# Kernel optimization log

Hardware: AMD Instinct MI355X
Metric: run time of the kernel (lower is better)

## Reference

```python
import jax, jax.numpy as jnp
import numpy as np


def setup_inputs() -> dict:
    key = jax.random.key(0)
    k1, k2, k3 = jax.random.split(key, 3)
    B, N, D = 16, 4096, 64
    q = jax.random.normal(k1, (B, N, D), dtype=jnp.float32)
    k = jax.random.normal(k2, (B, N, D), dtype=jnp.float32)
    v = jax.random.normal(k3, (B, N, D), dtype=jnp.float32)
    return {"q": q, "k": k, "v": v}


def reference(q, k, v):
    # attention = softmax(q @ k^T, axis=2)  (scale=None in the torch module,
    # dropout=0.0 is identity)
    scores = jnp.einsum("bnd,bmd->bnm", q, k)          # [B, N, N]
    attention = jax.nn.softmax(scores, axis=2)          # softmax over keys
    context = jnp.einsum("bnm,bmd->bnd", attention, v)  # [B, N, D]
    return (context, attention)
```

## Files before the change

kernel.cpp:

```cpp
#include <hip/hip_runtime.h>
#include <hip/hip_bf16.h>

typedef _Float16 half8 __attribute__((ext_vector_type(8)));
typedef _Float16 half4 __attribute__((ext_vector_type(4)));
typedef short short8 __attribute__((ext_vector_type(8)));
typedef short short4v __attribute__((ext_vector_type(4)));
typedef float f32x4 __attribute__((ext_vector_type(4)));

#define BATCH 16
#define SEQ   4096
#define DIM   64
#define KVB   64
#define NCH   (SEQ / KVB)
#define NSC   (NCH / 2)
#define EL_CH 4096
#define EL_SC 8192
#define EL_B  (NCH * EL_CH)
#define PHS   136

__device__ __forceinline__ short f2bf(float f) {
    unsigned u = __builtin_bit_cast(unsigned, f);
    u += 0x7FFF + ((u >> 16) & 1);
    return (short)(u >> 16);
}
__device__ __forceinline__ float bf2f(short h) {
    return __builtin_bit_cast(float, (unsigned)((unsigned short)h) << 16);
}

__device__ __forceinline__ void gld16(const void* g, void* l) {
    __builtin_amdgcn_global_load_lds(
        (const __attribute__((address_space(1))) unsigned int*)g,
        (__attribute__((address_space(3))) unsigned int*)l, 16, 0, 0);
}

__global__ __launch_bounds__(256) void preconvert(
    const float* __restrict__ k, const float* __restrict__ v,
    _Float16* __restrict__ kh, _Float16* __restrict__ vh)
{
    int f = blockIdx.x * 256 + threadIdx.x;
    int lane = f & 63;
    int sub  = (f >> 6) & 7;
    int ch   = (f >> 9) & 63;
    int bb   = (f >> 15) & 15;
    int isV  = f >> 19;
    int nf = sub >> 1, kk = sub & 1;
    size_t fo = (size_t)(f & ((1 << 19) - 1)) * 8;

    if (!isV) {
        int key = ch * 64 + nf * 16 + (lane & 15);
        int d0  = kk * 32 + (lane >> 4) * 8;
        const float* src = k + (((size_t)bb * SEQ + key) * DIM + d0);
        half8 h8;
        #pragma unroll
        for (int e = 0; e < 8; ++e) h8[e] = (_Float16)src[e];
        *(half8*)(kh + fo) = h8;
    } else {
        int kr0 = kk * 32 + (lane >> 4) * 8;
        int d   = nf * 16 + (lane & 15);
        const float* src = v + (((size_t)bb * SEQ + ch * 64 + kr0) * DIM + d);
        half8 h8;
        #pragma unroll
        for (int e = 0; e < 8; ++e) h8[e] = (_Float16)src[e * DIM];
        *(half8*)(vh + fo) = h8;
    }
}

__global__ __launch_bounds__(512, 2) void attn_main(
    const float* __restrict__ q, const _Float16* __restrict__ kh,
    const _Float16* __restrict__ vh, float* __restrict__ ctx,
    float* __restrict__ att)
{
    __shared__ __align__(16) _Float16 Kst[2][EL_SC];
    __shared__ __align__(16) _Float16 Vst[2][EL_SC];
    __shared__ __align__(16) _Float16 Ph[8][16][PHS];

    int id = blockIdx.x;
    int bb = (id & 7) + 8 * (id >> 8);
    int qt = (id >> 3) & 31;

    int tid = threadIdx.x;
    int w = tid >> 6, lane = tid & 63, li = lane & 15, h4 = lane >> 4;

    int qrow = qt * 128 + w * 16 + li;
    const float* qp = q + ((size_t)bb * SEQ + qrow) * DIM;
    half8 aq[2];
    #pragma unroll
    for (int kk = 0; kk < 2; ++kk)
        #pragma unroll
        for (int e = 0; e < 8; ++e)
            aq[kk][e] = (_Float16)qp[kk * 32 + h4 * 8 + e];

    const _Float16* khb = kh + (size_t)bb * EL_B;
    const _Float16* vvb = vh + (size_t)bb * EL_B;

    auto qkt = [&](const _Float16* base, f32x4* s) {
        const half8* k8 = (const half8*)base;
        #pragma unroll
        for (int kk = 0; kk < 2; ++kk)
            #pragma unroll
            for (int nf = 0; nf < 4; ++nf)
                s[nf] = __builtin_amdgcn_mfma_f32_16x16x32_f16(
                    k8[(nf * 2 + kk) * 64 + lane], aq[kk], s[nf], 0, 0, 0);
    };

    float ll = 0.f;

    auto stage_sc = [&](int buf, int sc) {
        const _Float16* g = khb + (size_t)sc * EL_SC + tid * 8;
        gld16(g,        &Kst[buf][w * 512]);
        gld16(g + 4096, &Kst[buf][4096 + w * 512]);
    };

    stage_sc(0, 0);
    for (int sc = 0; sc < NSC; ++sc) {
        int buf = sc & 1;
        if (sc + 1 < NSC) {
            stage_sc(buf ^ 1, sc + 1);
            asm volatile("s_waitcnt vmcnt(2)" ::: "memory");
        } else {
            asm volatile("s_waitcnt vmcnt(0)" ::: "memory");
        }
        __builtin_amdgcn_s_barrier();
        asm volatile("" ::: "memory");

        #pragma unroll
        for (int c2 = 0; c2 < 2; ++c2) {
            f32x4 s[4];
            #pragma unroll
            for (int nf = 0; nf < 4; ++nf) s[nf] = (f32x4){0.f, 0.f, 0.f, 0.f};
            qkt(&Kst[buf][c2 * EL_CH], s);
            float a = 0.f;
            #pragma unroll
            for (int nf = 0; nf < 4; ++nf)
                #pragma unroll
                for (int r = 0; r < 4; ++r)
                    a += __expf(s[nf][r]);
            ll += a;
        }

        asm volatile("" ::: "memory");
        __builtin_amdgcn_s_barrier();
    }

    ll += __shfl_xor(ll, 16);
    ll += __shfl_xor(ll, 32);
    float rl = 1.0f / ll;

    f32x4 acc[4];
    #pragma unroll
    for (int nf = 0; nf < 4; ++nf) acc[nf] = (f32x4){0.f, 0.f, 0.f, 0.f};

    float* attb = att + ((size_t)bb * SEQ + (size_t)qt * 128 + w * 16) * SEQ;

    auto stage_k2 = [&](int buf, int sc) {
        const _Float16* g = khb + (size_t)sc * EL_SC + tid * 8;
        gld16(g,        &Kst[buf][w * 512]);
        gld16(g + 4096, &Kst[buf][4096 + w * 512]);
    };
    auto stage_v2 = [&](int buf, int sc) {
        const _Float16* g = vvb + (size_t)sc * EL_SC + tid * 8;
        gld16(g,        &Vst[buf][w * 512]);
        gld16(g + 4096, &Vst[buf][4096 + w * 512]);
    };

    stage_k2(0, 0); stage_v2(0, 0);
    for (int sc = 0; sc < NSC; ++sc) {
        int buf = sc & 1;
        if (sc + 1 < NSC) {
            stage_k2(buf ^ 1, sc + 1);
            stage_v2(buf ^ 1, sc + 1);
            if (sc == 0) asm volatile("s_waitcnt vmcnt(4)"  ::: "memory");
            else         asm volatile("s_waitcnt vmcnt(12)" ::: "memory");
        } else {
            asm volatile("s_waitcnt vmcnt(8)" ::: "memory");
        }
        __builtin_amdgcn_s_barrier();
        asm volatile("" ::: "memory");

        f32x4 sA[4], sB[4];
        #pragma unroll
        for (int nf = 0; nf < 4; ++nf) {
            sA[nf] = (f32x4){0.f, 0.f, 0.f, 0.f};
            sB[nf] = (f32x4){0.f, 0.f, 0.f, 0.f};
        }
        qkt(&Kst[buf][0],     sA);
        qkt(&Kst[buf][EL_CH], sB);

        #pragma unroll
        for (int nf = 0; nf < 4; ++nf) {
            half4 pa, pb;
            #pragma unroll
            for (int r = 0; r < 4; ++r) {
                pa[r] = (_Float16)(__expf(sA[nf][r]) * rl);
                pb[r] = (_Float16)(__expf(sB[nf][r]) * rl);
            }
            *(half4*)&Ph[w][li][nf * 16 + h4 * 4]      = pa;
            *(half4*)&Ph[w][li][64 + nf * 16 + h4 * 4] = pb;
        }

        #pragma unroll
        for (int j = 0; j < 4; ++j) {
            int row = j * 4 + h4;
            half4 pa = *(const half4*)&Ph[w][row][li * 4];
            half4 pb = *(const half4*)&Ph[w][row][64 + li * 4];
            f32x4 va = { (float)pa[0], (float)pa[1], (float)pa[2], (float)pa[3] };
            f32x4 vb = { (float)pb[0], (float)pb[1], (float)pb[2], (float)pb[3] };
            float* dst = attb + (size_t)row * SEQ + sc * 128;
            __builtin_nontemporal_store(va, (f32x4*)(dst + li * 4));
            __builtin_nontemporal_store(vb, (f32x4*)(dst + 64 + li * 4));
        }

        const half8* v8 = (const half8*)&Vst[buf][0];
        #pragma unroll
        for (int kk = 0; kk < 4; ++kk) {
            half8 pa = *(const half8*)&Ph[w][li][kk * 32 + h4 * 8];
            #pragma unroll
            for (int nf = 0; nf < 4; ++nf)
                acc[nf] = __builtin_amdgcn_mfma_f32_16x16x32_f16(
                    pa, v8[(kk >> 1) * 512 + (nf * 2 + (kk & 1)) * 64 + lane],
                    acc[nf], 0, 0, 0);
        }

        asm volatile("" ::: "memory");
        __builtin_amdgcn_s_barrier();
    }

    float* ctxb = ctx + ((size_t)bb * SEQ + (size_t)qt * 128 + w * 16) * DIM;
    #pragma unroll
    for (int nf = 0; nf < 4; ++nf)
        #pragma unroll
        for (int r = 0; r < 4; ++r)
            __builtin_nontemporal_store(
                acc[nf][r], &ctxb[(size_t)(4 * h4 + r) * DIM + nf * 16 + li]);
}

__global__ __launch_bounds__(256) void attn_fallback(
    const float* __restrict__ q, const float* __restrict__ k,
    const float* __restrict__ v, float* __restrict__ ctx,
    float* __restrict__ att)
{
    __shared__ short K_hi[KVB][72];
    __shared__ short K_lo[KVB][72];
    __shared__ short V_lds[DIM][72];
    __shared__ short P_lds[4][16][72];

    int id = blockIdx.x;
    int bb = (id & 7) + 8 * (id >> 9);
    int qt = (id >> 3) & 63;
    int tid = threadIdx.x;
    int w = tid >> 6, lane = tid & 63, li = lane & 15, h4 = lane >> 4;

    int qrow = qt * 64 + w * 16 + li;
    const float* qp = q + ((size_t)bb * SEQ + qrow) * DIM;
    short8 aq[2], aql[2];
    #pragma unroll
    for (int kk = 0; kk < 2; ++kk)
        #pragma unroll
        for (int e = 0; e < 8; ++e) {
            float x = qp[kk * 32 + h4 * 8 + e];
            short h = f2bf(x);
            aq[kk][e] = h; aql[kk][e] = f2bf(x - bf2f(h));
        }

    float m[4], l[4];
    #pragma unroll
    for (int r = 0; r < 4; ++r) { m[r] = -3.0e38f; l[r] = 0.0f; }
    const float* kbase = k + (size_t)bb * SEQ * DIM;
    const float* vbase = v + (size_t)bb * SEQ * DIM;

    for (int ch = 0; ch < NCH; ++ch) {
        __syncthreads();
        const float4* kc = (const float4*)(kbase + (size_t)ch * KVB * DIM);
        #pragma unroll
        for (int j = 0; j < 4; ++j) {
            int f4 = j * 256 + tid; int key = f4 >> 4, d4 = f4 & 15;
            float4 val = kc[f4];
            short4v h4v, l4v;
            h4v[0]=f2bf(val.x); l4v[0]=f2bf(val.x-bf2f(h4v[0]));
            h4v[1]=f2bf(val.y); l4v[1]=f2bf(val.y-bf2f(h4v[1]));
            h4v[2]=f2bf(val.z); l4v[2]=f2bf(val.z-bf2f(h4v[2]));
            h4v[3]=f2bf(val.w); l4v[3]=f2bf(val.w-bf2f(h4v[3]));
            *(short4v*)&K_hi[key][d4*4] = h4v;
            *(short4v*)&K_lo[key][d4*4] = l4v;
        }
        __syncthreads();
        f32x4 s[4];
        #pragma unroll
        for (int nf = 0; nf < 4; ++nf) s[nf] = (f32x4){0.f,0.f,0.f,0.f};
        #pragma unroll
        for (int kk = 0; kk < 2; ++kk)
            #pragma unroll
            for (int nf = 0; nf < 4; ++nf) {
                short8 kbv = *(const short8*)&K_hi[nf*16+li][kk*32+h4*8];
                short8 klv = *(const short8*)&K_lo[nf*16+li][kk*32+h4*8];
                s[nf] = __builtin_amdgcn_mfma_f32_16x16x32_bf16(aq[kk],  kbv, s[nf],0,0,0);
                s[nf] = __builtin_amdgcn_mfma_f32_16x16x32_bf16(aq[kk],  klv, s[nf],0,0,0);
                s[nf] = __builtin_amdgcn_mfma_f32_16x16x32_bf16(aql[kk], kbv, s[nf],0,0,0);
            }
        #pragma unroll
        for (int r = 0; r < 4; ++r) {
            float cmax = fmaxf(fmaxf(s[0][r],s[1][r]), fmaxf(s[2][r],s[3][r]));
            #pragma unroll
            for (int off = 1; off < 16; off <<= 1) cmax = fmaxf(cmax, __shfl_xor(cmax, off));
            float mnew = fmaxf(m[r], cmax);
            float cs = __expf(s[0][r]-mnew)+__expf(s[1][r]-mnew)+__expf(s[2][r]-mnew)+__expf(s[3][r]-mnew);
            #pragma unroll
            for (int off = 1; off < 16; off <<= 1) cs += __shfl_xor(cs, off);
            l[r] = l[r]*__expf(m[r]-mnew) + cs; m[r] = mnew;
        }
    }
    float rl[4];
    #pragma unroll
    for (int r = 0; r < 4; ++r) rl[r] = 1.0f / l[r];

    f32x4 acc[4];
    #pragma unroll
    for (int nf = 0; nf < 4; ++nf) acc[nf] = (f32x4){0.f,0.f,0.f,0.f};
    float* attb = att + ((size_t)bb * SEQ + (size_t)qt * 64 + w * 16) * SEQ;

    for (int ch = 0; ch < NCH; ++ch) {
        __syncthreads();
        const float4* kc = (const float4*)(kbase + (size_t)ch * KVB * DIM);
        #pragma unroll
        for (int j = 0; j < 4; ++j) {
            int f4 = j * 256 + tid; int key = f4 >> 4, d4 = f4 & 15;
            float4 val = kc[f4];
            short4v h4v, l4v;
            h4v[0]=f2bf(val.x); l4v[0]=f2bf(val.x-bf2f(h4v[0]));
            h4v[1]=f2bf(val.y); l4v[1]=f2bf(val.y-bf2f(h4v[1]));
            h4v[2]=f2bf(val.z); l4v[2]=f2bf(val.z-bf2f(h4v[2]));
            h4v[3]=f2bf(val.w); l4v[3]=f2bf(val.w-bf2f(h4v[3]));
            *(short4v*)&K_hi[key][d4*4] = h4v;
            *(short4v*)&K_lo[key][d4*4] = l4v;
        }
        {
            int key = tid & 63, dblk = (tid >> 6) * 16;
            const float* vc = vbase + ((size_t)ch * KVB + key) * DIM + dblk;
            #pragma unroll
            for (int j = 0; j < 4; ++j) {
                float4 val = *(const float4*)(vc + j * 4);
                V_lds[dblk+j*4+0][key]=f2bf(val.x); V_lds[dblk+j*4+1][key]=f2bf(val.y);
                V_lds[dblk+j*4+2][key]=f2bf(val.z); V_lds[dblk+j*4+3][key]=f2bf(val.w);
            }
        }
        __syncthreads();
        f32x4 s[4];
        #pragma unroll
        for (int nf = 0; nf < 4; ++nf) s[nf] = (f32x4){0.f,0.f,0.f,0.f};
        #pragma unroll
        for (int kk = 0; kk < 2; ++kk)
            #pragma unroll
            for (int nf = 0; nf < 4; ++nf) {
                short8 kbv = *(const short8*)&K_hi[nf*16+li][kk*32+h4*8];
                short8 klv = *(const short8*)&K_lo[nf*16+li][kk*32+h4*8];
                s[nf] = __builtin_amdgcn_mfma_f32_16x16x32_bf16(aq[kk],  kbv, s[nf],0,0,0);
                s[nf] = __builtin_amdgcn_mfma_f32_16x16x32_bf16(aq[kk],  klv, s[nf],0,0,0);
                s[nf] = __builtin_amdgcn_mfma_f32_16x16x32_bf16(aql[kk], kbv, s[nf],0,0,0);
            }
        #pragma unroll
        for (int nf = 0; nf < 4; ++nf)
            #pragma unroll
            for (int r = 0; r < 4; ++r) {
                float p = __expf(s[nf][r] - m[r]) * rl[r];
                __builtin_nontemporal_store(p, &attb[(size_t)(4*h4+r)*SEQ + ch*KVB + nf*16 + li]);
                P_lds[w][4*h4+r][nf*16+li] = f2bf(p);
            }
        #pragma unroll
        for (int kk = 0; kk < 2; ++kk) {
            short8 pa = *(const short8*)&P_lds[w][li][kk*32+h4*8];
            #pragma unroll
            for (int nf = 0; nf < 4; ++nf) {
                short8 vbv = *(const short8*)&V_lds[nf*16+li][kk*32+h4*8];
                acc[nf] = __builtin_amdgcn_mfma_f32_16x16x32_bf16(pa, vbv, acc[nf],0,0,0);
            }
        }
    }
    float* ctxb = ctx + ((size_t)bb * SEQ + (size_t)qt * 64 + w * 16) * DIM;
    #pragma unroll
    for (int nf = 0; nf < 4; ++nf)
        #pragma unroll
        for (int r = 0; r < 4; ++r)
            __builtin_nontemporal_store(acc[nf][r], &ctxb[(size_t)(4*h4+r)*DIM + nf*16 + li]);
}

extern "C" void kernel_launch(void* const* d_in, const int* in_sizes, int n_in,
                              void* d_out, int out_size, void* d_ws, size_t ws_size,
                              hipStream_t stream) {
    const float* q = (const float*)d_in[0];
    const float* k = (const float*)d_in[1];
    const float* v = (const float*)d_in[2];
    float* ctx = (float*)d_out;
    float* att = (float*)d_out + (size_t)BATCH * SEQ * DIM;

    const size_t t_el = (size_t)BATCH * EL_B;
    const size_t need = 2 * t_el * 2;

    if (ws_size >= need) {
        _Float16* kh = (_Float16*)d_ws;
        _Float16* vh = kh + t_el;
        preconvert<<<4096, 256, 0, stream>>>(k, v, kh, vh);
        attn_main<<<512, 512, 0, stream>>>(q, kh, vh, ctx, att);
    } else {
        attn_fallback<<<BATCH * (SEQ / 64), 256, 0, stream>>>(q, k, v, ctx, att);
    }
}
```

Before: 282.1 us.

## Batch attention stores across chunk pairs and widen pass-1 K staging

Pass 1 now stages 256 keys per iteration (four chunks) instead of 128, which halves the number of barriers and waits. In pass 2 the P tile is double-slotted in LDS, and the attention-matrix writes are deferred by one pair and issued as 256-column, full-row stores. Those stores overlap with the next chunk's loads and MFMAs, and vmcnt waits are retuned so the pending stores are counted. All buffers move into one aliased LDS pool; LDS stays about the same size, but the deferred-store scheme relies on exact vmcnt accounting.

Result: faster. 261.8 us (-7.2%).

```diff
diff --git a/kernel.cpp b/kernel.cpp
--- a/kernel.cpp
+++ b/kernel.cpp
@@ -12,11 +12,13 @@
 #define DIM   64
 #define KVB   64
 #define NCH   (SEQ / KVB)
-#define NSC   (NCH / 2)
+#define NP2   32
+#define NP1   16
 #define EL_CH 4096
 #define EL_SC 8192
+#define EL_P1 16384
 #define EL_B  (NCH * EL_CH)
-#define PHS   136
+#define PHS   264
 
 __device__ __forceinline__ short f2bf(float f) {
     unsigned u = __builtin_bit_cast(unsigned, f);
@@ -70,9 +72,7 @@
     const _Float16* __restrict__ vh, float* __restrict__ ctx,
     float* __restrict__ att)
 {
-    __shared__ __align__(16) _Float16 Kst[2][EL_SC];
-    __shared__ __align__(16) _Float16 Vst[2][EL_SC];
-    __shared__ __align__(16) _Float16 Ph[8][16][PHS];
+    __shared__ __align__(16) _Float16 POOL[66560];
 
     int id = blockIdx.x;
     int bb = (id & 7) + 8 * (id >> 8);
@@ -80,6 +80,8 @@
 
     int tid = threadIdx.x;
     int w = tid >> 6, lane = tid & 63, li = lane & 15, h4 = lane >> 4;
+
+    _Float16* Ph = POOL + 32768 + w * (16 * PHS);
 
     int qrow = qt * 128 + w * 16 + li;
     const float* qp = q + ((size_t)bb * SEQ + qrow) * DIM;
@@ -105,18 +107,21 @@
 
     float ll = 0.f;
 
-    auto stage_sc = [&](int buf, int sc) {
-        const _Float16* g = khb + (size_t)sc * EL_SC + tid * 8;
-        gld16(g,        &Kst[buf][w * 512]);
-        gld16(g + 4096, &Kst[buf][4096 + w * 512]);
+    auto stage_p1 = [&](int buf, int sc) {
+        const _Float16* g = khb + (size_t)sc * EL_P1 + tid * 8;
+        _Float16* d = POOL + buf * EL_P1;
+        gld16(g,         d + w * 512);
+        gld16(g + 4096,  d + 4096  + w * 512);
+        gld16(g + 8192,  d + 8192  + w * 512);
+        gld16(g + 12288, d + 12288 + w * 512);
     };
 
-    stage_sc(0, 0);
-    for (int sc = 0; sc < NSC; ++sc) {
+    stage_p1(0, 0);
+    for (int sc = 0; sc < NP1; ++sc) {
         int buf = sc & 1;
-        if (sc + 1 < NSC) {
-            stage_sc(buf ^ 1, sc + 1);
-            asm volatile("s_waitcnt vmcnt(2)" ::: "memory");
+        if (sc + 1 < NP1) {
+            stage_p1(buf ^ 1, sc + 1);
+            asm volatile("s_waitcnt vmcnt(4)" ::: "memory");
         } else {
             asm volatile("s_waitcnt vmcnt(0)" ::: "memory");
         }
@@ -124,11 +129,11 @@
         asm volatile("" ::: "memory");
 
         #pragma unroll
-        for (int c2 = 0; c2 < 2; ++c2) {
+        for (int c4 = 0; c4 < 4; ++c4) {
             f32x4 s[4];
             #pragma unroll
             for (int nf = 0; nf < 4; ++nf) s[nf] = (f32x4){0.f, 0.f, 0.f, 0.f};
-            qkt(&Kst[buf][c2 * EL_CH], s);
+            qkt(POOL + buf * EL_P1 + c4 * EL_CH, s);
             float a = 0.f;
             #pragma unroll
             for (int nf = 0; nf < 4; ++nf)
@@ -154,38 +159,52 @@
 
     auto stage_k2 = [&](int buf, int sc) {
         const _Float16* g = khb + (size_t)sc * EL_SC + tid * 8;
-        gld16(g,        &Kst[buf][w * 512]);
-        gld16(g + 4096, &Kst[buf][4096 + w * 512]);
+        _Float16* d = POOL + buf * EL_SC;
+        gld16(g,        d + w * 512);
+        gld16(g + 4096, d + 4096 + w * 512);
     };
     auto stage_v2 = [&](int buf, int sc) {
         const _Float16* g = vvb + (size_t)sc * EL_SC + tid * 8;
-        gld16(g,        &Vst[buf][w * 512]);
-        gld16(g + 4096, &Vst[buf][4096 + w * 512]);
+        _Float16* d = POOL + 16384 + buf * EL_SC;
+        gld16(g,        d + w * 512);
+        gld16(g + 4096, d + 4096 + w * 512);
     };
+    auto store_pair = [&](int p) {
+        #pragma unroll
+        for (int row = 0; row < 16; ++row) {
+            half4 ph = *(const half4*)&Ph[row * PHS + lane * 4];
+            f32x4 pv = { (float)ph[0], (float)ph[1], (float)ph[2], (float)ph[3] };
+            __builtin_nontemporal_store(
+                pv, (f32x4*)(attb + (size_t)row * SEQ + p * 256 + lane * 4));
+        }
+    };
 
     stage_k2(0, 0); stage_v2(0, 0);
-    for (int sc = 0; sc < NSC; ++sc) {
+    for (int sc = 0; sc < NP2; ++sc) {
         int buf = sc & 1;
-        if (sc + 1 < NSC) {
+        if (sc + 1 < NP2) {
             stage_k2(buf ^ 1, sc + 1);
             stage_v2(buf ^ 1, sc + 1);
-            if (sc == 0) asm volatile("s_waitcnt vmcnt(4)"  ::: "memory");
-            else         asm volatile("s_waitcnt vmcnt(12)" ::: "memory");
-        } else {
-            asm volatile("s_waitcnt vmcnt(8)" ::: "memory");
-        }
+        }
+        if (sc >= 2 && (sc & 1) == 0) store_pair(sc / 2 - 1);
+
+        if (sc < 2)            asm volatile("s_waitcnt vmcnt(4)"  ::: "memory");
+        else if (sc + 1 < NP2) asm volatile("s_waitcnt vmcnt(20)" ::: "memory");
+        else                   asm volatile("s_waitcnt vmcnt(16)" ::: "memory");
         __builtin_amdgcn_s_barrier();
         asm volatile("" ::: "memory");
 
+        const _Float16* kc = POOL + buf * EL_SC;
         f32x4 sA[4], sB[4];
         #pragma unroll
         for (int nf = 0; nf < 4; ++nf) {
             sA[nf] = (f32x4){0.f, 0.f, 0.f, 0.f};
             sB[nf] = (f32x4){0.f, 0.f, 0.f, 0.f};
         }
-        qkt(&Kst[buf][0],     sA);
-        qkt(&Kst[buf][EL_CH], sB);
-
+        qkt(kc,         sA);
+        qkt(kc + EL_CH, sB);
+
+        int slot = (sc & 1) * 128;
         #pragma unroll
         for (int nf = 0; nf < 4; ++nf) {
             half4 pa, pb;
@@ -194,26 +213,14 @@
                 pa[r] = (_Float16)(__expf(sA[nf][r]) * rl);
                 pb[r] = (_Float16)(__expf(sB[nf][r]) * rl);
             }
-            *(half4*)&Ph[w][li][nf * 16 + h4 * 4]      = pa;
-            *(half4*)&Ph[w][li][64 + nf * 16 + h4 * 4] = pb;
-        }
-
-        #pragma unroll
-        for (int j = 0; j < 4; ++j) {
-            int row = j * 4 + h4;
-            half4 pa = *(const half4*)&Ph[w][row][li * 4];
-            half4 pb = *(const half4*)&Ph[w][row][64 + li * 4];
-            f32x4 va = { (float)pa[0], (float)pa[1], (float)pa[2], (float)pa[3] };
-            f32x4 vb = { (float)pb[0], (float)pb[1], (float)pb[2], (float)pb[3] };
-            float* dst = attb + (size_t)row * SEQ + sc * 128;
-            __builtin_nontemporal_store(va, (f32x4*)(dst + li * 4));
-            __builtin_nontemporal_store(vb, (f32x4*)(dst + 64 + li * 4));
-        }
-
-        const half8* v8 = (const half8*)&Vst[buf][0];
+            *(half4*)&Ph[li * PHS + slot + nf * 16 + h4 * 4]      = pa;
+            *(half4*)&Ph[li * PHS + slot + 64 + nf * 16 + h4 * 4] = pb;
+        }
+
+        const half8* v8 = (const half8*)(POOL + 16384 + buf * EL_SC);
         #pragma unroll
         for (int kk = 0; kk < 4; ++kk) {
-            half8 pa = *(const half8*)&Ph[w][li][kk * 32 + h4 * 8];
+            half8 pa = *(const half8*)&Ph[li * PHS + slot + kk * 32 + h4 * 8];
             #pragma unroll
             for (int nf = 0; nf < 4; ++nf)
                 acc[nf] = __builtin_amdgcn_mfma_f32_16x16x32_f16(
@@ -224,6 +231,7 @@
         asm volatile("" ::: "memory");
         __builtin_amdgcn_s_barrier();
     }
+    store_pair(NP2 / 2 - 1);
 
     float* ctxb = ctx + ((size_t)bb * SEQ + (size_t)qt * 128 + w * 16) * DIM;
     #pragma unroll
```
